# Performance work log

Hardware: AMD Instinct MI355X
Metric: run time of the kernel (lower is better)

Reference implementation:

```python
import jax, jax.numpy as jnp
import numpy as np

N = 50000   # nodes
E = 800000  # edges
F = 64      # edge_feat_dim == input node dim
H0, H1 = 128, 64  # hidden_dims
OUT = 2
EPS = 1e-5


def _glorot(key, shape):
    limit = float(np.sqrt(6.0 / (shape[0] + shape[1])))
    return jax.random.uniform(key, shape, minval=-limit, maxval=limit, dtype=jnp.float32)


def _layer_norm(h, g, b):
    m = jnp.mean(h, axis=-1, keepdims=True)
    v = jnp.var(h, axis=-1, keepdims=True)
    return (h - m) * jax.lax.rsqrt(v + EPS) * g + b


def setup_inputs() -> dict:
    key = jax.random.key(0)
    ks = jax.random.split(key, 10)
    x = jax.random.normal(ks[0], (N, F), dtype=jnp.float32)
    edge_index = jax.random.randint(ks[1], (2, E), 0, N, dtype=jnp.int64)
    edge_attr = jax.random.normal(ks[2], (E, F), dtype=jnp.float32)
    # conv layer 0: Linear(F + F -> H0); conv layer 1: Linear(H0 + F -> H1)
    W0 = _glorot(ks[3], (F + F, H0)); b0 = jnp.zeros((H0,), jnp.float32)
    W1 = _glorot(ks[4], (H0 + F, H1)); b1 = jnp.zeros((H1,), jnp.float32)
    g0 = jnp.ones((H0,), jnp.float32); be0 = jnp.zeros((H0,), jnp.float32)
    g1 = jnp.ones((H1,), jnp.float32); be1 = jnp.zeros((H1,), jnp.float32)
    # classifier: Linear(2*H1 -> H1) -> ReLU -> Linear(H1 -> OUT)
    Wc0 = _glorot(ks[5], (2 * H1, H1)); bc0 = jnp.zeros((H1,), jnp.float32)
    Wc1 = _glorot(ks[6], (H1, OUT)); bc1 = jnp.zeros((OUT,), jnp.float32)
    return dict(x=x, edge_index=edge_index, edge_attr=edge_attr,
                W0=W0, b0=b0, g0=g0, be0=be0,
                W1=W1, b1=b1, g1=g1, be1=be1,
                Wc0=Wc0, bc0=bc0, Wc1=Wc1, bc1=bc1)


def reference(x, edge_index, edge_attr, W0, b0, g0, be0, W1, b1, g1, be1, Wc0, bc0, Wc1, bc1):
    src, dst = edge_index[0], edge_index[1]
    # scatter-mean of edge_attr per destination node (same for both layers,
    # since edge_attr never changes -> compute once)
    agg_sum = jax.ops.segment_sum(edge_attr, dst, num_segments=N)  # [N, F]
    cnt = jax.ops.segment_sum(jnp.ones((E, 1), x.dtype), dst, num_segments=N)
    agg = agg_sum / jnp.maximum(cnt, 1.0)
    # layer 0: cat -> linear -> relu -> layernorm (dropout is identity at eval)
    h = jax.nn.relu(jnp.concatenate([x, agg], axis=-1) @ W0 + b0)
    h = _layer_norm(h, g0, be0)
    # layer 1
    h = jax.nn.relu(jnp.concatenate([h, agg], axis=-1) @ W1 + b1)
    z = _layer_norm(h, g1, be1)  # [N, H1]
    # edge classifier: gather src/dst embeddings, concat, MLP
    edge_emb = jnp.concatenate([z[src], z[dst]], axis=-1)  # [E, 2*H1]
    hidden = jax.nn.relu(edge_emb @ Wc0 + bc0)
    return hidden @ Wc1 + bc1  # [E, OUT]
```

## Files before the change

### kernel.cpp

```cpp
#include <hip/hip_runtime.h>
#include <hip/hip_bf16.h>

#define N_NODES 50000
#define N_EDGES 800000
#define EPS 1e-5f
#define SCAN_BLOCKS 49

typedef __attribute__((ext_vector_type(8))) short short8;
typedef __attribute__((ext_vector_type(4))) float f32x4;

static __device__ __forceinline__ unsigned short f2bf(float f) {
  union { float f; unsigned u; } v; v.f = f;
  const unsigned r = v.u + 0x7FFF + ((v.u >> 16) & 1);
  return (unsigned short)(r >> 16);
}

__global__ void __launch_bounds__(256) k_prepw(
    const float* __restrict__ W0, const float* __restrict__ W1,
    const float* __restrict__ Wc0,
    unsigned short* __restrict__ W0T, unsigned short* __restrict__ W1T,
    unsigned short* __restrict__ Wc0T, int* __restrict__ cnt) {
  const int idx = blockIdx.x * 256 + threadIdx.x;
  if (idx < 128 * 128) {
    const int n = idx >> 7, k = idx & 127;
    W0T[idx] = f2bf(W0[k * 128 + n]);
  }
  if (idx < 64 * 192) {
    const int n = idx / 192, k = idx - n * 192;
    W1T[idx] = f2bf(W1[k * 64 + n]);
  }
  if (idx < 64 * 128) {
    const int n = idx >> 7, k = idx & 127;
    Wc0T[idx] = f2bf(Wc0[k * 64 + n]);
  }
  for (int i = idx; i < N_NODES; i += 64 * 256) cnt[i] = 0;
}

__global__ void k_count(const int* __restrict__ ei, int* __restrict__ cnt) {
  const int e = blockIdx.x * blockDim.x + threadIdx.x;
  if (e < N_EDGES) atomicAdd(&cnt[ei[N_EDGES + e]], 1);
}

__global__ void __launch_bounds__(256) k_scan_blk(const int* __restrict__ cnt,
                                                  int* __restrict__ starts,
                                                  int* __restrict__ bsum) {
  __shared__ int lds[256];
  const int t = threadIdx.x, b = blockIdx.x;
  const int base = b * 1024 + t * 4;
  int c0 = 0, c1 = 0, c2 = 0, c3 = 0;
  if (base + 3 < N_NODES) {
    const int4 c = *(const int4*)(cnt + base);
    c0 = c.x; c1 = c.y; c2 = c.z; c3 = c.w;
  } else {
    if (base + 0 < N_NODES) c0 = cnt[base + 0];
    if (base + 1 < N_NODES) c1 = cnt[base + 1];
    if (base + 2 < N_NODES) c2 = cnt[base + 2];
    if (base + 3 < N_NODES) c3 = cnt[base + 3];
  }
  const int s = c0 + c1 + c2 + c3;
  lds[t] = s;
  __syncthreads();
  for (int off = 1; off < 256; off <<= 1) {
    const int v = (t >= off) ? lds[t - off] : 0;
    __syncthreads();
    lds[t] += v;
    __syncthreads();
  }
  int run = lds[t] - s;
  if (t == 255) bsum[b] = lds[255];
  const int o0 = run; run += c0;
  const int o1 = run; run += c1;
  const int o2 = run; run += c2;
  const int o3 = run;
  if (base + 3 < N_NODES) {
    *(int4*)(starts + base) = make_int4(o0, o1, o2, o3);
  } else {
    if (base + 0 < N_NODES) starts[base + 0] = o0;
    if (base + 1 < N_NODES) starts[base + 1] = o1;
    if (base + 2 < N_NODES) starts[base + 2] = o2;
    if (base + 3 < N_NODES) starts[base + 3] = o3;
  }
}

__global__ void __launch_bounds__(256) k_scan_add(int* __restrict__ starts,
                                                  int* __restrict__ pos,
                                                  const int* __restrict__ bsum) {
  __shared__ int s_off;
  const int t = threadIdx.x, b = blockIdx.x;
  if (t < 64) {
    int v = (t < b) ? bsum[t] : 0;
    for (int o = 32; o; o >>= 1) v += __shfl_xor(v, o);
    if (t == 0) s_off = v;
  }
  __syncthreads();
  const int off = s_off;
  const int base = b * 1024 + t * 4;
  if (base + 3 < N_NODES) {
    int4 v = *(const int4*)(starts + base);
    v.x += off; v.y += off; v.z += off; v.w += off;
    *(int4*)(starts + base) = v;
    *(int4*)(pos + base) = v;
  } else {
    for (int i = 0; i < 4; ++i)
      if (base + i < N_NODES) {
        const int v = starts[base + i] + off;
        starts[base + i] = v;
        pos[base + i] = v;
      }
  }
  if (b == 0 && t == 0) starts[N_NODES] = N_EDGES;
}

__global__ void k_place(const int* __restrict__ ei, int* __restrict__ pos,
                        int* __restrict__ csr) {
  const int e = blockIdx.x * blockDim.x + threadIdx.x;
  if (e < N_EDGES) {
    const int d = ei[N_EDGES + e];
    const int slot = atomicAdd(&pos[d], 1);
    csr[slot] = e;
  }
}

__global__ void __launch_bounds__(256) k_gather(const float* __restrict__ ea,
                                                const int* __restrict__ csr,
                                                const int* __restrict__ starts,
                                                unsigned short* __restrict__ aggb) {
  const int lane = threadIdx.x & 63;
  const int wv = threadIdx.x >> 6;
  const int wstride = gridDim.x * 4;
  for (int n = blockIdx.x * 4 + wv; n < N_NODES; n += wstride) {
    const int s0 = starts[n], s1 = starts[n + 1];
    float sum = 0.0f;
    int i = s0;
    for (; i + 3 < s1; i += 4) {
      const int e0 = csr[i], e1 = csr[i + 1], e2 = csr[i + 2], e3 = csr[i + 3];
      const float a0 = ea[(size_t)e0 * 64 + lane];
      const float a1 = ea[(size_t)e1 * 64 + lane];
      const float a2 = ea[(size_t)e2 * 64 + lane];
      const float a3 = ea[(size_t)e3 * 64 + lane];
      sum += (a0 + a1) + (a2 + a3);
    }
    for (; i < s1; ++i) sum += ea[(size_t)csr[i] * 64 + lane];
    const int deg = s1 - s0;
    aggb[(size_t)n * 64 + lane] = f2bf(sum / (float)max(deg, 1));
  }
}

__global__ void __launch_bounds__(256) k_nodes(
    const float* __restrict__ x, const unsigned short* __restrict__ aggb,
    const unsigned short* __restrict__ W0T, const float* __restrict__ b0,
    const float* __restrict__ g0, const float* __restrict__ be0,
    const unsigned short* __restrict__ W1T, const float* __restrict__ b1,
    const float* __restrict__ g1, const float* __restrict__ be1,
    unsigned short* __restrict__ zb) {
  __shared__ char A0[64 * 256];
  __shared__ char A1[64 * 384];
  __shared__ float red0[64][4], red1[64][4];

  const int t = threadIdx.x;
  const int lane = t & 63;
  const int w = t >> 6;
  const int m = lane & 15;
  const int g = lane >> 4;
  const int nbase = blockIdx.x * 64;

  {
    const int row = t >> 2, seg = t & 3;
    const int node = nbase + row;
    const int swz = (row & 7) << 4;
    unsigned short h[16];
    if (node < N_NODES) {
      const float4* xr = (const float4*)(x + (size_t)node * 64 + seg * 16);
#pragma unroll
      for (int i = 0; i < 4; ++i) {
        const float4 v = xr[i];
        h[4 * i + 0] = f2bf(v.x); h[4 * i + 1] = f2bf(v.y);
        h[4 * i + 2] = f2bf(v.z); h[4 * i + 3] = f2bf(v.w);
      }
    } else {
#pragma unroll
      for (int i = 0; i < 16; ++i) h[i] = 0;
    }
    uint4 lo, hi;
    unsigned* lp = (unsigned*)&lo;
    unsigned* hp = (unsigned*)&hi;
#pragma unroll
    for (int i = 0; i < 4; ++i) lp[i] = (unsigned)h[2 * i] | ((unsigned)h[2 * i + 1] << 16);
#pragma unroll
    for (int i = 0; i < 4; ++i) hp[i] = (unsigned)h[8 + 2 * i] | ((unsigned)h[8 + 2 * i + 1] << 16);
    *(uint4*)(A0 + row * 256 + ((seg * 32) ^ swz)) = lo;
    *(uint4*)(A0 + row * 256 + ((seg * 32 + 16) ^ swz)) = hi;
    uint4 a0v = make_uint4(0, 0, 0, 0), a1v = make_uint4(0, 0, 0, 0);
    if (node < N_NODES) {
      const uint4* ap = (const uint4*)(aggb + (size_t)node * 64 + seg * 16);
      a0v = ap[0]; a1v = ap[1];
    }
    *(uint4*)(A0 + row * 256 + ((128 + seg * 32) ^ swz)) = a0v;
    *(uint4*)(A0 + row * 256 + ((128 + seg * 32 + 16) ^ swz)) = a1v;
    *(uint4*)(A1 + row * 384 + ((256 + seg * 32) ^ swz)) = a0v;
    *(uint4*)(A1 + row * 384 + ((256 + seg * 32 + 16) ^ swz)) = a1v;
  }

  short8 B0[4][2];
#pragma unroll
  for (int ks = 0; ks < 4; ++ks)
#pragma unroll
    for (int nt = 0; nt < 2; ++nt) {
      const int n = w * 32 + nt * 16 + m;
      B0[ks][nt] = *(const short8*)(W0T + n * 128 + ks * 32 + 8 * g);
    }

  __syncthreads();

  f32x4 acc0[4][2];
#pragma unroll
  for (int mt = 0; mt < 4; ++mt)
#pragma unroll
    for (int nt = 0; nt < 2; ++nt) acc0[mt][nt] = (f32x4){0.f, 0.f, 0.f, 0.f};
#pragma unroll
  for (int ks = 0; ks < 4; ++ks)
#pragma unroll
    for (int mt = 0; mt < 4; ++mt) {
      const int row = 16 * mt + m;
      const short8 a = *(const short8*)(A0 + row * 256 + ((ks * 64 + g * 16) ^ ((row & 7) << 4)));
      acc0[mt][0] = __builtin_amdgcn_mfma_f32_16x16x32_bf16(a, B0[ks][0], acc0[mt][0], 0, 0, 0);
      acc0[mt][1] = __builtin_amdgcn_mfma_f32_16x16x32_bf16(a, B0[ks][1], acc0[mt][1], 0, 0, 0);
    }

  float b0c[2], g0c[2], be0c[2];
#pragma unroll
  for (int nt = 0; nt < 2; ++nt) {
    const int c = w * 32 + nt * 16 + m;
    b0c[nt] = b0[c]; g0c[nt] = g0[c]; be0c[nt] = be0[c];
  }
  float ps1[4][4], ps2[4][4];
#pragma unroll
  for (int mt = 0; mt < 4; ++mt)
#pragma unroll
    for (int q = 0; q < 4; ++q) {
      const float v0 = fmaxf(acc0[mt][0][q] + b0c[0], 0.f);
      const float v1 = fmaxf(acc0[mt][1][q] + b0c[1], 0.f);
      ps1[mt][q] = v0 + v1;
      ps2[mt][q] = v0 * v0 + v1 * v1;
    }
#pragma unroll
  for (int mask = 1; mask <= 8; mask <<= 1)
#pragma unroll
    for (int mt = 0; mt < 4; ++mt)
#pragma unroll
      for (int q = 0; q < 4; ++q) {
        ps1[mt][q] += __shfl_xor(ps1[mt][q], mask);
        ps2[mt][q] += __shfl_xor(ps2[mt][q], mask);
      }
  if (m == 0) {
#pragma unroll
    for (int mt = 0; mt < 4; ++mt)
#pragma unroll
      for (int q = 0; q < 4; ++q) {
        const int row = 16 * mt + 4 * g + q;
        red0[row][w] = ps1[mt][q];
        red1[row][w] = ps2[mt][q];
      }
  }
  __syncthreads();

#pragma unroll
  for (int mt = 0; mt < 4; ++mt)
#pragma unroll
    for (int q = 0; q < 4; ++q) {
      const int row = 16 * mt + 4 * g + q;
      const float4 r0 = *(const float4*)red0[row];
      const float4 r1 = *(const float4*)red1[row];
      const float S1 = (r0.x + r0.y) + (r0.z + r0.w);
      const float S2 = (r1.x + r1.y) + (r1.z + r1.w);
      const float mean = S1 * (1.0f / 128.0f);
      const float var = S2 * (1.0f / 128.0f) - mean * mean;
      const float inv = rsqrtf(var + EPS);
#pragma unroll
      for (int nt = 0; nt < 2; ++nt) {
        const float v = fmaxf(acc0[mt][nt][q] + b0c[nt], 0.f);
        const float o = (v - mean) * inv * g0c[nt] + be0c[nt];
        const int col = w * 32 + nt * 16 + m;
        *(unsigned short*)(A1 + row * 384 + ((2 * col) ^ ((row & 7) << 4))) = f2bf(o);
      }
    }

  short8 B1[6];
  {
    const int n = w * 16 + m;
#pragma unroll
    for (int ks = 0; ks < 6; ++ks)
      B1[ks] = *(const short8*)(W1T + n * 192 + ks * 32 + 8 * g);
  }
  __syncthreads();

  f32x4 acc1[4];
#pragma unroll
  for (int mt = 0; mt < 4; ++mt) acc1[mt] = (f32x4){0.f, 0.f, 0.f, 0.f};
#pragma unroll
  for (int ks = 0; ks < 6; ++ks)
#pragma unroll
    for (int mt = 0; mt < 4; ++mt) {
      const int row = 16 * mt + m;
      const short8 a = *(const short8*)(A1 + row * 384 + ((ks * 64 + g * 16) ^ ((row & 7) << 4)));
      acc1[mt] = __builtin_amdgcn_mfma_f32_16x16x32_bf16(a, B1[ks], acc1[mt], 0, 0, 0);
    }

  const int c1i = w * 16 + m;
  const float b1c = b1[c1i], g1c = g1[c1i], be1c = be1[c1i];
  float qs1[4][4], qs2[4][4];
#pragma unroll
  for (int mt = 0; mt < 4; ++mt)
#pragma unroll
    for (int q = 0; q < 4; ++q) {
      const float v = fmaxf(acc1[mt][q] + b1c, 0.f);
      qs1[mt][q] = v;
      qs2[mt][q] = v * v;
    }
#pragma unroll
  for (int mask = 1; mask <= 8; mask <<= 1)
#pragma unroll
    for (int mt = 0; mt < 4; ++mt)
#pragma unroll
      for (int q = 0; q < 4; ++q) {
        qs1[mt][q] += __shfl_xor(qs1[mt][q], mask);
        qs2[mt][q] += __shfl_xor(qs2[mt][q], mask);
      }
  if (m == 0) {
#pragma unroll
    for (int mt = 0; mt < 4; ++mt)
#pragma unroll
      for (int q = 0; q < 4; ++q) {
        const int row = 16 * mt + 4 * g + q;
        red0[row][w] = qs1[mt][q];
        red1[row][w] = qs2[mt][q];
      }
  }
  __syncthreads();
#pragma unroll
  for (int mt = 0; mt < 4; ++mt)
#pragma unroll
    for (int q = 0; q < 4; ++q) {
      const int row = 16 * mt + 4 * g + q;
      const int node = nbase + row;
      const float4 r0 = *(const float4*)red0[row];
      const float4 r1 = *(const float4*)red1[row];
      const float S1 = (r0.x + r0.y) + (r0.z + r0.w);
      const float S2 = (r1.x + r1.y) + (r1.z + r1.w);
      const float mean = S1 * (1.0f / 64.0f);
      const float var = S2 * (1.0f / 64.0f) - mean * mean;
      const float inv = rsqrtf(var + EPS);
      const float v = fmaxf(acc1[mt][q] + b1c, 0.f);
      const float o = (v - mean) * inv * g1c + be1c;
      if (node < N_NODES) zb[(size_t)node * 64 + c1i] = f2bf(o);
    }
}

__global__ void __launch_bounds__(256) k_cls_mfma(
    const unsigned short* __restrict__ zb, const int* __restrict__ ei,
    const unsigned short* __restrict__ Wc0T, const float* __restrict__ bc0,
    const float* __restrict__ Wc1, const float* __restrict__ bc1,
    float* __restrict__ out) {
  const int t = threadIdx.x;
  const int lane = t & 63;
  const int w = t >> 6;
  const int m = lane & 15;
  const int g = lane >> 4;

  short8 bfrag[4][4];
#pragma unroll
  for (int ks = 0; ks < 4; ++ks)
#pragma unroll
    for (int nt = 0; nt < 4; ++nt)
      bfrag[ks][nt] = *(const short8*)(Wc0T + (nt * 16 + m) * 128 + ks * 32 + 8 * g);
  float wc1v0[4], wc1v1[4], bc0v[4];
#pragma unroll
  for (int nt = 0; nt < 4; ++nt) {
    const int j = nt * 16 + m;
    wc1v0[nt] = Wc1[j * 2 + 0];
    wc1v1[nt] = Wc1[j * 2 + 1];
    bc0v[nt] = bc0[j];
  }
  const float ob0 = bc1[0], ob1 = bc1[1];

  const int gstride = gridDim.x * 4;
  for (int grp = blockIdx.x * 4 + w; grp < N_EDGES / 16; grp += gstride) {
    const int ebase = grp * 16;
    const int e = ebase + m;
    const int s = ei[e], d = ei[N_EDGES + e];
    const short8 a0 = *(const short8*)(zb + (size_t)s * 64 + 8 * g);
    const short8 a1 = *(const short8*)(zb + (size_t)s * 64 + 32 + 8 * g);
    const short8 a2 = *(const short8*)(zb + (size_t)d * 64 + 8 * g);
    const short8 a3 = *(const short8*)(zb + (size_t)d * 64 + 32 + 8 * g);

    f32x4 acc0 = {0.f, 0.f, 0.f, 0.f}, acc1 = acc0, acc2 = acc0, acc3 = acc0;
    acc0 = __builtin_amdgcn_mfma_f32_16x16x32_bf16(a0, bfrag[0][0], acc0, 0, 0, 0);
    acc1 = __builtin_amdgcn_mfma_f32_16x16x32_bf16(a0, bfrag[0][1], acc1, 0, 0, 0);
    acc2 = __builtin_amdgcn_mfma_f32_16x16x32_bf16(a0, bfrag[0][2], acc2, 0, 0, 0);
    acc3 = __builtin_amdgcn_mfma_f32_16x16x32_bf16(a0, bfrag[0][3], acc3, 0, 0, 0);
    acc0 = __builtin_amdgcn_mfma_f32_16x16x32_bf16(a1, bfrag[1][0], acc0, 0, 0, 0);
    acc1 = __builtin_amdgcn_mfma_f32_16x16x32_bf16(a1, bfrag[1][1], acc1, 0, 0, 0);
    acc2 = __builtin_amdgcn_mfma_f32_16x16x32_bf16(a1, bfrag[1][2], acc2, 0, 0, 0);
    acc3 = __builtin_amdgcn_mfma_f32_16x16x32_bf16(a1, bfrag[1][3], acc3, 0, 0, 0);
    acc0 = __builtin_amdgcn_mfma_f32_16x16x32_bf16(a2, bfrag[2][0], acc0, 0, 0, 0);
    acc1 = __builtin_amdgcn_mfma_f32_16x16x32_bf16(a2, bfrag[2][1], acc1, 0, 0, 0);
    acc2 = __builtin_amdgcn_mfma_f32_16x16x32_bf16(a2, bfrag[2][2], acc2, 0, 0, 0);
    acc3 = __builtin_amdgcn_mfma_f32_16x16x32_bf16(a2, bfrag[2][3], acc3, 0, 0, 0);
    acc0 = __builtin_amdgcn_mfma_f32_16x16x32_bf16(a3, bfrag[3][0], acc0, 0, 0, 0);
    acc1 = __builtin_amdgcn_mfma_f32_16x16x32_bf16(a3, bfrag[3][1], acc1, 0, 0, 0);
    acc2 = __builtin_amdgcn_mfma_f32_16x16x32_bf16(a3, bfrag[3][2], acc2, 0, 0, 0);
    acc3 = __builtin_amdgcn_mfma_f32_16x16x32_bf16(a3, bfrag[3][3], acc3, 0, 0, 0);

    float p0[4], p1[4];
#pragma unroll
    for (int r = 0; r < 4; ++r) {
      const float h0v = fmaxf(acc0[r] + bc0v[0], 0.f);
      const float h1v = fmaxf(acc1[r] + bc0v[1], 0.f);
      const float h2v = fmaxf(acc2[r] + bc0v[2], 0.f);
      const float h3v = fmaxf(acc3[r] + bc0v[3], 0.f);
      p0[r] = h0v * wc1v0[0] + h1v * wc1v0[1] + h2v * wc1v0[2] + h3v * wc1v0[3];
      p1[r] = h0v * wc1v1[0] + h1v * wc1v1[1] + h2v * wc1v1[2] + h3v * wc1v1[3];
    }
#pragma unroll
    for (int mask = 1; mask <= 8; mask <<= 1)
#pragma unroll
      for (int r = 0; r < 4; ++r) {
        p0[r] += __shfl_xor(p0[r], mask);
        p1[r] += __shfl_xor(p1[r], mask);
      }
    const int eout = ebase + g * 4;
#pragma unroll
    for (int r = 0; r < 4; ++r) {
      if (m == 2 * r) out[(size_t)(eout + r) * 2 + 0] = p0[r] + ob0;
      if (m == 2 * r + 1) out[(size_t)(eout + r) * 2 + 1] = p1[r] + ob1;
    }
  }
}

extern "C" void kernel_launch(void* const* d_in, const int* in_sizes, int n_in,
                              void* d_out, int out_size, void* d_ws, size_t ws_size,
                              hipStream_t stream) {
  const float* x   = (const float*)d_in[0];
  const int*   ei  = (const int*)d_in[1];
  const float* ea  = (const float*)d_in[2];
  const float* W0  = (const float*)d_in[3];
  const float* b0  = (const float*)d_in[4];
  const float* g0  = (const float*)d_in[5];
  const float* be0 = (const float*)d_in[6];
  const float* W1  = (const float*)d_in[7];
  const float* b1  = (const float*)d_in[8];
  const float* g1  = (const float*)d_in[9];
  const float* be1 = (const float*)d_in[10];
  const float* Wc0 = (const float*)d_in[11];
  const float* bc0 = (const float*)d_in[12];
  const float* Wc1 = (const float*)d_in[13];
  const float* bc1 = (const float*)d_in[14];
  float* out = (float*)d_out;

  char* base = (char*)d_ws;
  unsigned short* zb   = (unsigned short*)base;
  unsigned short* aggb = zb + (size_t)N_NODES * 64;
  unsigned short* W0T  = aggb + (size_t)N_NODES * 64;
  unsigned short* W1T  = W0T + 128 * 128;
  unsigned short* Wc0T = W1T + 64 * 192;
  int* cnt    = (int*)(Wc0T + 64 * 128);
  int* starts = cnt + N_NODES;
  int* pos    = starts + N_NODES + 4;
  int* bsum   = pos + N_NODES;
  int* csr    = bsum + 64;

  k_prepw<<<64, 256, 0, stream>>>(W0, W1, Wc0, W0T, W1T, Wc0T, cnt);
  k_count<<<(N_EDGES + 255) / 256, 256, 0, stream>>>(ei, cnt);
  k_scan_blk<<<SCAN_BLOCKS, 256, 0, stream>>>(cnt, starts, bsum);
  k_scan_add<<<SCAN_BLOCKS, 256, 0, stream>>>(starts, pos, bsum);
  k_place<<<(N_EDGES + 255) / 256, 256, 0, stream>>>(ei, pos, csr);
  k_gather<<<12500, 256, 0, stream>>>(ea, csr, starts, aggb);
  k_nodes<<<(N_NODES + 63) / 64, 256, 0, stream>>>(x, aggb, W0T, b0, g0, be0,
                                                   W1T, b1, g1, be1, zb);
  k_cls_mfma<<<2048, 256, 0, stream>>>(zb, ei, Wc0T, bc0, Wc1, bc1, out);
}
```

Baseline: 213.8 us.

## Fuse CSR build and aggregation into one cooperative kernel with grid syncs

Replaces the six launches (weight prep, count, two scan passes, place, gather) with a single cooperative kernel of 1024 blocks that separates the phases with grid.sync(). This removes per-launch overhead and the idle gaps between small kernels. The gather loop is also unrolled to eight edges per iteration to keep more loads in flight, and the classifier grid size is raised from 2048 to 12500 blocks. The fixed grid gives the gather and the atomic phases less parallelism than before, and each grid barrier has its own cost.

```diff
diff --git a/kernel.cpp b/kernel.cpp
--- a/kernel.cpp
+++ b/kernel.cpp
@@ -1,10 +1,14 @@
 #include <hip/hip_runtime.h>
 #include <hip/hip_bf16.h>
+#include <hip/hip_cooperative_groups.h>
+
+namespace cg = cooperative_groups;
 
 #define N_NODES 50000
 #define N_EDGES 800000
 #define EPS 1e-5f
 #define SCAN_BLOCKS 49
+#define BUILD_BLOCKS 1024
 
 typedef __attribute__((ext_vector_type(8))) short short8;
 typedef __attribute__((ext_vector_type(4))) float f32x4;
@@ -15,134 +19,141 @@
   return (unsigned short)(r >> 16);
 }
 
-__global__ void __launch_bounds__(256) k_prepw(
+__global__ void __launch_bounds__(256) k_build(
     const float* __restrict__ W0, const float* __restrict__ W1,
     const float* __restrict__ Wc0,
     unsigned short* __restrict__ W0T, unsigned short* __restrict__ W1T,
-    unsigned short* __restrict__ Wc0T, int* __restrict__ cnt) {
-  const int idx = blockIdx.x * 256 + threadIdx.x;
-  if (idx < 128 * 128) {
+    unsigned short* __restrict__ Wc0T,
+    const int* __restrict__ ei, const float* __restrict__ ea,
+    int* __restrict__ cnt, int* __restrict__ starts, int* __restrict__ pos,
+    int* __restrict__ bsum, int* __restrict__ csr,
+    unsigned short* __restrict__ aggb) {
+  cg::grid_group grid = cg::this_grid();
+  __shared__ int lds[256];
+  __shared__ int s_off;
+  const int t = threadIdx.x, b = blockIdx.x;
+  const int gid = b * 256 + t;
+  const int nthreads = BUILD_BLOCKS * 256;
+
+  for (int idx = gid; idx < 128 * 128; idx += nthreads) {
     const int n = idx >> 7, k = idx & 127;
     W0T[idx] = f2bf(W0[k * 128 + n]);
   }
-  if (idx < 64 * 192) {
+  for (int idx = gid; idx < 64 * 192; idx += nthreads) {
     const int n = idx / 192, k = idx - n * 192;
     W1T[idx] = f2bf(W1[k * 64 + n]);
   }
-  if (idx < 64 * 128) {
+  for (int idx = gid; idx < 64 * 128; idx += nthreads) {
     const int n = idx >> 7, k = idx & 127;
     Wc0T[idx] = f2bf(Wc0[k * 64 + n]);
   }
-  for (int i = idx; i < N_NODES; i += 64 * 256) cnt[i] = 0;
-}
-
-__global__ void k_count(const int* __restrict__ ei, int* __restrict__ cnt) {
-  const int e = blockIdx.x * blockDim.x + threadIdx.x;
-  if (e < N_EDGES) atomicAdd(&cnt[ei[N_EDGES + e]], 1);
-}
-
-__global__ void __launch_bounds__(256) k_scan_blk(const int* __restrict__ cnt,
-                                                  int* __restrict__ starts,
-                                                  int* __restrict__ bsum) {
-  __shared__ int lds[256];
-  const int t = threadIdx.x, b = blockIdx.x;
-  const int base = b * 1024 + t * 4;
-  int c0 = 0, c1 = 0, c2 = 0, c3 = 0;
-  if (base + 3 < N_NODES) {
-    const int4 c = *(const int4*)(cnt + base);
-    c0 = c.x; c1 = c.y; c2 = c.z; c3 = c.w;
-  } else {
-    if (base + 0 < N_NODES) c0 = cnt[base + 0];
-    if (base + 1 < N_NODES) c1 = cnt[base + 1];
-    if (base + 2 < N_NODES) c2 = cnt[base + 2];
-    if (base + 3 < N_NODES) c3 = cnt[base + 3];
-  }
-  const int s = c0 + c1 + c2 + c3;
-  lds[t] = s;
-  __syncthreads();
-  for (int off = 1; off < 256; off <<= 1) {
-    const int v = (t >= off) ? lds[t - off] : 0;
+  for (int i = gid; i < N_NODES; i += nthreads) cnt[i] = 0;
+  grid.sync();
+
+  for (int e = gid; e < N_EDGES; e += nthreads)
+    atomicAdd(&cnt[ei[N_EDGES + e]], 1);
+  grid.sync();
+
+  if (b < SCAN_BLOCKS) {
+    const int base = b * 1024 + t * 4;
+    int c0 = 0, c1 = 0, c2 = 0, c3 = 0;
+    if (base + 3 < N_NODES) {
+      const int4 c = *(const int4*)(cnt + base);
+      c0 = c.x; c1 = c.y; c2 = c.z; c3 = c.w;
+    } else {
+      if (base + 0 < N_NODES) c0 = cnt[base + 0];
+      if (base + 1 < N_NODES) c1 = cnt[base + 1];
+      if (base + 2 < N_NODES) c2 = cnt[base + 2];
+      if (base + 3 < N_NODES) c3 = cnt[base + 3];
+    }
+    const int s = c0 + c1 + c2 + c3;
+    lds[t] = s;
     __syncthreads();
-    lds[t] += v;
+    for (int off = 1; off < 256; off <<= 1) {
+      const int v = (t >= off) ? lds[t - off] : 0;
+      __syncthreads();
+      lds[t] += v;
+      __syncthreads();
+    }
+    int run = lds[t] - s;
+    if (t == 255) bsum[b] = lds[255];
+    const int o0 = run; run += c0;
+    const int o1 = run; run += c1;
+    const int o2 = run; run += c2;
+    const int o3 = run;
+    if (base + 3 < N_NODES) {
+      *(int4*)(starts + base) = make_int4(o0, o1, o2, o3);
+    } else {
+      if (base + 0 < N_NODES) starts[base + 0] = o0;
+      if (base + 1 < N_NODES) starts[base + 1] = o1;
+      if (base + 2 < N_NODES) starts[base + 2] = o2;
+      if (base + 3 < N_NODES) starts[base + 3] = o3;
+    }
+  }
+  grid.sync();
+
+  if (b < SCAN_BLOCKS) {
+    if (t < 64) {
+      int v = (t < b) ? bsum[t] : 0;
+      for (int o = 32; o; o >>= 1) v += __shfl_xor(v, o);
+      if (t == 0) s_off = v;
+    }
     __syncthreads();
-  }
-  int run = lds[t] - s;
-  if (t == 255) bsum[b] = lds[255];
-  const int o0 = run; run += c0;
-  const int o1 = run; run += c1;
-  const int o2 = run; run += c2;
-  const int o3 = run;
-  if (base + 3 < N_NODES) {
-    *(int4*)(starts + base) = make_int4(o0, o1, o2, o3);
-  } else {
-    if (base + 0 < N_NODES) starts[base + 0] = o0;
-    if (base + 1 < N_NODES) starts[base + 1] = o1;
-    if (base + 2 < N_NODES) starts[base + 2] = o2;
-    if (base + 3 < N_NODES) starts[base + 3] = o3;
-  }
-}
-
-__global__ void __launch_bounds__(256) k_scan_add(int* __restrict__ starts,
-                                                  int* __restrict__ pos,
-                                                  const int* __restrict__ bsum) {
-  __shared__ int s_off;
-  const int t = threadIdx.x, b = blockIdx.x;
-  if (t < 64) {
-    int v = (t < b) ? bsum[t] : 0;
-    for (int o = 32; o; o >>= 1) v += __shfl_xor(v, o);
-    if (t == 0) s_off = v;
-  }
-  __syncthreads();
-  const int off = s_off;
-  const int base = b * 1024 + t * 4;
-  if (base + 3 < N_NODES) {
-    int4 v = *(const int4*)(starts + base);
-    v.x += off; v.y += off; v.z += off; v.w += off;
-    *(int4*)(starts + base) = v;
-    *(int4*)(pos + base) = v;
-  } else {
-    for (int i = 0; i < 4; ++i)
-      if (base + i < N_NODES) {
-        const int v = starts[base + i] + off;
-        starts[base + i] = v;
-        pos[base + i] = v;
-      }
-  }
-  if (b == 0 && t == 0) starts[N_NODES] = N_EDGES;
-}
-
-__global__ void k_place(const int* __restrict__ ei, int* __restrict__ pos,
-                        int* __restrict__ csr) {
-  const int e = blockIdx.x * blockDim.x + threadIdx.x;
-  if (e < N_EDGES) {
+    const int off = s_off;
+    const int base = b * 1024 + t * 4;
+    if (base + 3 < N_NODES) {
+      int4 v = *(const int4*)(starts + base);
+      v.x += off; v.y += off; v.z += off; v.w += off;
+      *(int4*)(starts + base) = v;
+      *(int4*)(pos + base) = v;
+    } else {
+      for (int i = 0; i < 4; ++i)
+        if (base + i < N_NODES) {
+          const int v = starts[base + i] + off;
+          starts[base + i] = v;
+          pos[base + i] = v;
+        }
+    }
+    if (b == 0 && t == 0) starts[N_NODES] = N_EDGES;
+  }
+  grid.sync();
+
+  for (int e = gid; e < N_EDGES; e += nthreads) {
     const int d = ei[N_EDGES + e];
     const int slot = atomicAdd(&pos[d], 1);
     csr[slot] = e;
   }
-}
-
-__global__ void __launch_bounds__(256) k_gather(const float* __restrict__ ea,
-                                                const int* __restrict__ csr,
-                                                const int* __restrict__ starts,
-                                                unsigned short* __restrict__ aggb) {
-  const int lane = threadIdx.x & 63;
-  const int wv = threadIdx.x >> 6;
-  const int wstride = gridDim.x * 4;
-  for (int n = blockIdx.x * 4 + wv; n < N_NODES; n += wstride) {
-    const int s0 = starts[n], s1 = starts[n + 1];
-    float sum = 0.0f;
-    int i = s0;
-    for (; i + 3 < s1; i += 4) {
-      const int e0 = csr[i], e1 = csr[i + 1], e2 = csr[i + 2], e3 = csr[i + 3];
-      const float a0 = ea[(size_t)e0 * 64 + lane];
-      const float a1 = ea[(size_t)e1 * 64 + lane];
-      const float a2 = ea[(size_t)e2 * 64 + lane];
-      const float a3 = ea[(size_t)e3 * 64 + lane];
-      sum += (a0 + a1) + (a2 + a3);
-    }
-    for (; i < s1; ++i) sum += ea[(size_t)csr[i] * 64 + lane];
-    const int deg = s1 - s0;
-    aggb[(size_t)n * 64 + lane] = f2bf(sum / (float)max(deg, 1));
+  grid.sync();
+
+  {
+    const int lane = t & 63;
+    const int wv = t >> 6;
+    const int wstride = BUILD_BLOCKS * 4;
+    for (int n = b * 4 + wv; n < N_NODES; n += wstride) {
+      const int s0 = starts[n], s1 = starts[n + 1];
+      float sum = 0.0f;
+      int i = s0;
+      for (; i + 7 < s1; i += 8) {
+        int e[8];
+#pragma unroll
+        for (int j = 0; j < 8; ++j) e[j] = csr[i + j];
+        float a[8];
+#pragma unroll
+        for (int j = 0; j < 8; ++j) a[j] = ea[(size_t)e[j] * 64 + lane];
+        sum += ((a[0] + a[1]) + (a[2] + a[3])) + ((a[4] + a[5]) + (a[6] + a[7]));
+      }
+      for (; i + 3 < s1; i += 4) {
+        const int e0 = csr[i], e1 = csr[i + 1], e2 = csr[i + 2], e3 = csr[i + 3];
+        const float a0 = ea[(size_t)e0 * 64 + lane];
+        const float a1 = ea[(size_t)e1 * 64 + lane];
+        const float a2 = ea[(size_t)e2 * 64 + lane];
+        const float a3 = ea[(size_t)e3 * 64 + lane];
+        sum += (a0 + a1) + (a2 + a3);
+      }
+      for (; i < s1; ++i) sum += ea[(size_t)csr[i] * 64 + lane];
+      const int deg = s1 - s0;
+      aggb[(size_t)n * 64 + lane] = f2bf(sum / (float)max(deg, 1));
+    }
   }
 }
 
@@ -469,13 +480,16 @@
   int* bsum   = pos + N_NODES;
   int* csr    = bsum + 64;
 
-  k_prepw<<<64, 256, 0, stream>>>(W0, W1, Wc0, W0T, W1T, Wc0T, cnt);
-  k_count<<<(N_EDGES + 255) / 256, 256, 0, stream>>>(ei, cnt);
-  k_scan_blk<<<SCAN_BLOCKS, 256, 0, stream>>>(cnt, starts, bsum);
-  k_scan_add<<<SCAN_BLOCKS, 256, 0, stream>>>(starts, pos, bsum);
-  k_place<<<(N_EDGES + 255) / 256, 256, 0, stream>>>(ei, pos, csr);
-  k_gather<<<12500, 256, 0, stream>>>(ea, csr, starts, aggb);
+  void* args[] = {
+    (void*)&W0, (void*)&W1, (void*)&Wc0,
+    (void*)&W0T, (void*)&W1T, (void*)&Wc0T,
+    (void*)&ei, (void*)&ea,
+    (void*)&cnt, (void*)&starts, (void*)&pos,
+    (void*)&bsum, (void*)&csr, (void*)&aggb
+  };
+  hipLaunchCooperativeKernel((void*)k_build, dim3(BUILD_BLOCKS), dim3(256),
+                             args, 0, stream);
   k_nodes<<<(N_NODES + 63) / 64, 256, 0, stream>>>(x, aggb, W0T, b0, g0, be0,
                                                    W1T, b1, g1, be1, zb);
-  k_cls_mfma<<<2048, 256, 0, stream>>>(zb, ei, Wc0T, bc0, Wc1, bc1, out);
+  k_cls_mfma<<<12500, 256, 0, stream>>>(zb, ei, Wc0T, bc0, Wc1, bc1, out);
 }
```

Result: slower. 784.4 us (+266.9%).
